# Kernel tuning notes

Hardware: AMD Instinct MI355X
Metric: run time of the kernel (lower is better)

Reference implementation:

```python
import jax, jax.numpy as jnp
import numpy as np

B, N = 4, 1024            # batches, atoms per structure
IN_CH, OUT_CH = 16, 16
N_BASIS = 16
MAX_RADIUS = 3.5
BOX_L = 19.7              # cubic lattice constant -> ~24 neighbors/atom
GAMMA = MAX_RADIUS / N_BASIS
N_NORM = 24.0             # avg neighbor count, out /= sqrt(n_norm)


def _build_periodic_edges(seed=0):
    rng = np.random.default_rng(seed)
    pos = rng.uniform(0.0, BOX_L, (B, N, 3)).astype(np.float32)
    shifts = BOX_L * np.array([[i, j, k] for i in (-1, 0, 1)
                               for j in (-1, 0, 1) for k in (-1, 0, 1)],
                              dtype=np.float32)
    src_l, dst_l, vec_l = [], [], []
    r2 = MAX_RADIUS * MAX_RADIUS
    for z in range(B):
        p = pos[z]
        for s in shifts:  # 27 periodic images, chunked to keep memory small
            diff = (p[None, :, :] + s[None, None, :]) - p[:, None, :]  # [a,b,3] = image_b - a
            d2 = (diff * diff).sum(-1)
            a_idx, b_idx = np.nonzero(d2 < r2)
            dst_l.append((z * N + a_idx).astype(np.int32))
            src_l.append((z * N + b_idx).astype(np.int32))
            vec_l.append(diff[a_idx, b_idx])
    edge_src = np.concatenate(src_l)
    edge_dst = np.concatenate(dst_l)
    edge_vec = np.concatenate(vec_l).astype(np.float32)
    # original zeroes self-image displacements with |r| < 1e-10
    self_mask = np.linalg.norm(edge_vec, axis=-1) < 1e-10
    edge_vec[self_mask] = 0.0
    return edge_src, edge_dst, edge_vec


def setup_inputs() -> dict:
    key = jax.random.key(0)
    k1, k2 = jax.random.split(key)
    edge_src, edge_dst, edge_vec = _build_periodic_edges()
    x = jax.random.normal(k1, (B * N, IN_CH), dtype=jnp.float32)
    W = jax.random.normal(k2, (N_BASIS + 3, OUT_CH, IN_CH), dtype=jnp.float32) * 0.1
    return {
        "x": x,
        "W": W,
        "edge_vec": jnp.asarray(edge_vec),
        "edge_src": jnp.asarray(edge_src),
        "edge_dst": jnp.asarray(edge_dst),
    }


def reference(x, W, edge_vec, edge_src, edge_dst):
    # per-edge kernel features: gaussian radial basis + unit direction
    r = jnp.linalg.norm(edge_vec, axis=-1, keepdims=True)            # [E,1]
    centers = jnp.linspace(0.0, MAX_RADIUS, N_BASIS, dtype=x.dtype)
    basis = jnp.exp(-((r - centers) / GAMMA) ** 2)                   # [E,nb]
    rhat = jnp.where(r > 1e-10, edge_vec / jnp.maximum(r, 1e-10), 0.0)
    feat = jnp.concatenate([basis, rhat], axis=-1)                   # [E,nb+3]
    # per-edge kernel eval (kernels = self.kernel(radius) in the original)
    K = jnp.einsum('ef,foi->eoi', feat, W)                           # [E,out,in]
    # per-edge matvec + scatter-add over destination atoms
    msg = jnp.einsum('eoi,ei->eo', K, x[edge_src])                   # [E,out]
    out = jax.ops.segment_sum(msg, edge_dst, num_segments=x.shape[0])
    out = out / jnp.sqrt(jnp.asarray(N_NORM, x.dtype))               # n_norm ** 0.5
    return out.reshape(B, N, OUT_CH)
```

## Files before the change

kernel.cpp:

```cpp
#include <hip/hip_runtime.h>
#include <math.h>

#define IN_CH 16
#define OUT_CH 16
#define N_BASIS 16
#define N_FEAT 19
#define Y_STRIDE (N_FEAT * OUT_CH)
#define GAMMA_INV (16.0f / 3.5f)
#define CENTER_STEP (3.5f / 15.0f)
#define INV_SQRT_NNORM 0.20412414523193154f

__global__ __launch_bounds__(320) void precompute_y(
    const float* __restrict__ x, const float* __restrict__ W,
    float* __restrict__ y, float* __restrict__ out, int n_atoms) {
  __shared__ float xs[IN_CH];
  const int a = blockIdx.x;
  const int t = threadIdx.x;
  if (t < IN_CH) {
    xs[t] = x[a * IN_CH + t];
    out[a * OUT_CH + t] = 0.0f;
  }
  __syncthreads();
  if (t < Y_STRIDE) {
    const float4* w4 = (const float4*)(W + t * IN_CH);
    float acc = 0.f;
#pragma unroll
    for (int q = 0; q < 4; ++q) {
      float4 w = w4[q];
      acc += w.x * xs[4 * q + 0] + w.y * xs[4 * q + 1] +
             w.z * xs[4 * q + 2] + w.w * xs[4 * q + 3];
    }
    y[(size_t)a * Y_STRIDE + t] = acc;
  }
}

__global__ __launch_bounds__(256) void edge_scatter(
    const float* __restrict__ y, const float* __restrict__ edge_vec,
    const int* __restrict__ edge_src, const int* __restrict__ edge_dst,
    float* __restrict__ out, int E) {
  __shared__ float feat[16][N_FEAT];
  __shared__ float msg[16][OUT_CH];
  __shared__ int dsts[16];

  const int t = threadIdx.x;
  const int eg = t >> 4;
  const int o = t & 15;
  const int e = blockIdx.x * 16 + eg;
  const bool valid = (e < E);

  float vx = 0.f, vy = 0.f, vz = 0.f;
  int src = 0;
  if (valid) {
    vx = edge_vec[3 * e + 0];
    vy = edge_vec[3 * e + 1];
    vz = edge_vec[3 * e + 2];
    src = edge_src[e];
    if (o == 0) dsts[eg] = edge_dst[e];
  } else if (o == 0) {
    dsts[eg] = -1 - eg;
  }
  const float r = sqrtf(vx * vx + vy * vy + vz * vz);

  const float tt = (r - CENTER_STEP * (float)o) * GAMMA_INV;
  feat[eg][o] = __expf(-tt * tt);
  if (o < 3) {
    const float inv = (r > 1e-10f) ? (1.0f / r) : 0.0f;
    const float comp = (o == 0) ? vx : ((o == 1) ? vy : vz);
    feat[eg][N_BASIS + o] = comp * inv;
  }
  __syncthreads();

  float acc = 0.f;
  if (valid) {
    const float* __restrict__ yrow = y + (size_t)src * Y_STRIDE + o;
#pragma unroll
    for (int f = 0; f < N_FEAT; ++f) acc += feat[eg][f] * yrow[f * OUT_CH];
  }
  msg[eg][o] = acc;
  __syncthreads();

  const int mydst = dsts[eg];
  int leader = eg;
#pragma unroll
  for (int j = 0; j < 16; ++j) {
    if (dsts[j] == mydst) { leader = j; break; }
  }
  if (leader == eg && mydst >= 0) {
    float total = 0.f;
#pragma unroll
    for (int j = 0; j < 16; ++j) {
      if (j >= eg && dsts[j] == mydst) total += msg[j][o];
    }
    atomicAdd(&out[mydst * OUT_CH + o], total * INV_SQRT_NNORM);
  }
}

__global__ __launch_bounds__(256) void edge_direct(
    const float* __restrict__ x, const float* __restrict__ W,
    const float* __restrict__ edge_vec, const int* __restrict__ edge_src,
    const int* __restrict__ edge_dst, float* __restrict__ out, int E) {
  __shared__ float Ws[N_FEAT * OUT_CH * IN_CH];
  __shared__ float feat[16][N_FEAT];
  __shared__ float xs[16][IN_CH];

  const int t = threadIdx.x;
  for (int i = t; i < N_FEAT * OUT_CH * IN_CH; i += 256) Ws[i] = W[i];

  const int eg = t >> 4;
  const int o = t & 15;
  const int e = blockIdx.x * 16 + eg;
  const bool valid = (e < E);

  float vx = 0.f, vy = 0.f, vz = 0.f;
  int src = 0, dst = 0;
  if (valid) {
    vx = edge_vec[3 * e + 0];
    vy = edge_vec[3 * e + 1];
    vz = edge_vec[3 * e + 2];
    src = edge_src[e];
    dst = edge_dst[e];
    xs[eg][o] = x[src * IN_CH + o];
  }
  const float r = sqrtf(vx * vx + vy * vy + vz * vz);
  const float tt = (r - CENTER_STEP * (float)o) * GAMMA_INV;
  feat[eg][o] = __expf(-tt * tt);
  if (o < 3) {
    const float inv = (r > 1e-10f) ? (1.0f / r) : 0.0f;
    const float comp = (o == 0) ? vx : ((o == 1) ? vy : vz);
    feat[eg][N_BASIS + o] = comp * inv;
  }
  __syncthreads();

  if (valid) {
    float acc = 0.f;
#pragma unroll
    for (int f = 0; f < N_FEAT; ++f) {
      const float* wrow = &Ws[(f * OUT_CH + o) * IN_CH];
      float dot = 0.f;
#pragma unroll
      for (int i = 0; i < IN_CH; ++i) dot += wrow[i] * xs[eg][i];
      acc += feat[eg][f] * dot;
    }
    atomicAdd(&out[dst * OUT_CH + o], acc * INV_SQRT_NNORM);
  }
}

extern "C" void kernel_launch(void* const* d_in, const int* in_sizes, int n_in,
                              void* d_out, int out_size, void* d_ws,
                              size_t ws_size, hipStream_t stream) {
  const float* x = (const float*)d_in[0];
  const float* W = (const float*)d_in[1];
  const float* edge_vec = (const float*)d_in[2];
  const int* edge_src = (const int*)d_in[3];
  const int* edge_dst = (const int*)d_in[4];
  float* out = (float*)d_out;

  const int E = in_sizes[3];
  const int n_atoms = in_sizes[0] / IN_CH;

  const size_t y_bytes = (size_t)n_atoms * Y_STRIDE * sizeof(float);
  const int edge_blocks = (E + 15) / 16;
  if (ws_size >= y_bytes) {
    float* y = (float*)d_ws;
    precompute_y<<<n_atoms, 320, 0, stream>>>(x, W, y, out, n_atoms);
    edge_scatter<<<edge_blocks, 256, 0, stream>>>(y, edge_vec, edge_src,
                                                  edge_dst, out, E);
  } else {
    hipMemsetAsync(out, 0, (size_t)out_size * sizeof(float), stream);
    edge_direct<<<edge_blocks, 256, 0, stream>>>(x, W, edge_vec, edge_src,
                                                 edge_dst, out, E);
  }
}
```

Before: 83.84 us.

## Transpose y to feature-contiguous padded layout and process 64 edges per block

Changes the precomputed per-atom y table from [feat][out] to [out][feat padded to 20], so each output thread reads its 19 feature coefficients as five float4 loads. The edge kernel now handles 64 edges per 256-thread block with coalesced staging of edge vectors and indices in shared memory. The scatter reduction merges consecutive runs of equal destination within the larger tile, so fewer atomics are issued. The cost is a y table that is about 5% larger and more shared memory per block. The run-merge loop assumes edges are grouped by destination to get the full atomic reduction.

```diff
diff --git a/kernel.cpp b/kernel.cpp
--- a/kernel.cpp
+++ b/kernel.cpp
@@ -5,14 +5,16 @@
 #define OUT_CH 16
 #define N_BASIS 16
 #define N_FEAT 19
-#define Y_STRIDE (N_FEAT * OUT_CH)
+#define YF 20
+#define Y_STRIDE (OUT_CH * YF)
 #define GAMMA_INV (16.0f / 3.5f)
 #define CENTER_STEP (3.5f / 15.0f)
 #define INV_SQRT_NNORM 0.20412414523193154f
+#define EPB 64
 
 __global__ __launch_bounds__(320) void precompute_y(
     const float* __restrict__ x, const float* __restrict__ W,
-    float* __restrict__ y, float* __restrict__ out, int n_atoms) {
+    float* __restrict__ y, float* __restrict__ out) {
   __shared__ float xs[IN_CH];
   const int a = blockIdx.x;
   const int t = threadIdx.x;
@@ -21,77 +23,94 @@
     out[a * OUT_CH + t] = 0.0f;
   }
   __syncthreads();
-  if (t < Y_STRIDE) {
-    const float4* w4 = (const float4*)(W + t * IN_CH);
-    float acc = 0.f;
+  const int o = t / YF;
+  const int f = t % YF;
+  float acc = 0.f;
+  if (f < N_FEAT) {
+    const float4* w4 = (const float4*)(W + (f * OUT_CH + o) * IN_CH);
 #pragma unroll
     for (int q = 0; q < 4; ++q) {
       float4 w = w4[q];
       acc += w.x * xs[4 * q + 0] + w.y * xs[4 * q + 1] +
              w.z * xs[4 * q + 2] + w.w * xs[4 * q + 3];
     }
-    y[(size_t)a * Y_STRIDE + t] = acc;
   }
+  y[(size_t)a * Y_STRIDE + t] = acc;
 }
 
 __global__ __launch_bounds__(256) void edge_scatter(
     const float* __restrict__ y, const float* __restrict__ edge_vec,
     const int* __restrict__ edge_src, const int* __restrict__ edge_dst,
     float* __restrict__ out, int E) {
-  __shared__ float feat[16][N_FEAT];
-  __shared__ float msg[16][OUT_CH];
-  __shared__ int dsts[16];
+  __shared__ float ev[EPB * 3];
+  __shared__ int srcs[EPB];
+  __shared__ int dsts[EPB];
+  __shared__ float feat[EPB][YF];
+  __shared__ float msg[EPB][OUT_CH];
 
   const int t = threadIdx.x;
-  const int eg = t >> 4;
-  const int o = t & 15;
-  const int e = blockIdx.x * 16 + eg;
-  const bool valid = (e < E);
+  const int e0 = blockIdx.x * EPB;
 
-  float vx = 0.f, vy = 0.f, vz = 0.f;
-  int src = 0;
-  if (valid) {
-    vx = edge_vec[3 * e + 0];
-    vy = edge_vec[3 * e + 1];
-    vz = edge_vec[3 * e + 2];
-    src = edge_src[e];
-    if (o == 0) dsts[eg] = edge_dst[e];
-  } else if (o == 0) {
-    dsts[eg] = -1 - eg;
+  if (t < EPB * 3) {
+    const int idx = e0 * 3 + t;
+    ev[t] = (idx < E * 3) ? edge_vec[idx] : 0.0f;
   }
-  const float r = sqrtf(vx * vx + vy * vy + vz * vz);
-
-  const float tt = (r - CENTER_STEP * (float)o) * GAMMA_INV;
-  feat[eg][o] = __expf(-tt * tt);
-  if (o < 3) {
-    const float inv = (r > 1e-10f) ? (1.0f / r) : 0.0f;
-    const float comp = (o == 0) ? vx : ((o == 1) ? vy : vz);
-    feat[eg][N_BASIS + o] = comp * inv;
+  if (t < EPB) {
+    srcs[t] = (e0 + t < E) ? edge_src[e0 + t] : 0;
+  } else if (t < 2 * EPB) {
+    const int s = t - EPB;
+    dsts[s] = (e0 + s < E) ? edge_dst[e0 + s] : (-1 - s);
   }
   __syncthreads();
 
-  float acc = 0.f;
-  if (valid) {
-    const float* __restrict__ yrow = y + (size_t)src * Y_STRIDE + o;
+  const int g = t >> 4;
+  const int o = t & 15;
+
 #pragma unroll
-    for (int f = 0; f < N_FEAT; ++f) acc += feat[eg][f] * yrow[f * OUT_CH];
+  for (int j = 0; j < 4; ++j) {
+    const int s = g + 16 * j;
+    const float vx = ev[3 * s + 0], vy = ev[3 * s + 1], vz = ev[3 * s + 2];
+    const float r = sqrtf(vx * vx + vy * vy + vz * vz);
+    const float tt = (r - CENTER_STEP * (float)o) * GAMMA_INV;
+    feat[s][o] = __expf(-tt * tt);
+    if (o < 3) {
+      const float inv = (r > 1e-10f) ? (1.0f / r) : 0.0f;
+      const float comp = (o == 0) ? vx : ((o == 1) ? vy : vz);
+      feat[s][N_BASIS + o] = comp * inv;
+    }
+    if (o == 3) feat[s][N_FEAT] = 0.0f;
   }
-  msg[eg][o] = acc;
   __syncthreads();
 
-  const int mydst = dsts[eg];
-  int leader = eg;
 #pragma unroll
-  for (int j = 0; j < 16; ++j) {
-    if (dsts[j] == mydst) { leader = j; break; }
+  for (int j = 0; j < 4; ++j) {
+    const int s = g + 16 * j;
+    float acc = 0.f;
+    if (e0 + s < E) {
+      const float4* yr = (const float4*)(y + ((size_t)srcs[s] * OUT_CH + o) * YF);
+      const float4* fr = (const float4*)(&feat[s][0]);
+#pragma unroll
+      for (int q = 0; q < 5; ++q) {
+        float4 yv = yr[q];
+        float4 fv = fr[q];
+        acc += yv.x * fv.x + yv.y * fv.y + yv.z * fv.z + yv.w * fv.w;
+      }
+    }
+    msg[s][o] = acc;
   }
-  if (leader == eg && mydst >= 0) {
-    float total = 0.f;
+  __syncthreads();
+
 #pragma unroll
-    for (int j = 0; j < 16; ++j) {
-      if (j >= eg && dsts[j] == mydst) total += msg[j][o];
+  for (int j = 0; j < 4; ++j) {
+    const int s = g + 16 * j;
+    const int d = dsts[s];
+    const bool tail = (s == EPB - 1) || (dsts[s + 1] != d);
+    if (tail && d >= 0) {
+      float tot = 0.f;
+      int q = s;
+      while (q >= 0 && dsts[q] == d) { tot += msg[q][o]; --q; }
+      atomicAdd(&out[d * OUT_CH + o], tot * INV_SQRT_NNORM);
     }
-    atomicAdd(&out[mydst * OUT_CH + o], total * INV_SQRT_NNORM);
   }
 }
 
@@ -159,15 +178,14 @@
   const int n_atoms = in_sizes[0] / IN_CH;
 
   const size_t y_bytes = (size_t)n_atoms * Y_STRIDE * sizeof(float);
-  const int edge_blocks = (E + 15) / 16;
   if (ws_size >= y_bytes) {
     float* y = (float*)d_ws;
-    precompute_y<<<n_atoms, 320, 0, stream>>>(x, W, y, out, n_atoms);
-    edge_scatter<<<edge_blocks, 256, 0, stream>>>(y, edge_vec, edge_src,
-                                                  edge_dst, out, E);
+    precompute_y<<<n_atoms, 320, 0, stream>>>(x, W, y, out);
+    edge_scatter<<<(E + EPB - 1) / EPB, 256, 0, stream>>>(y, edge_vec, edge_src,
+                                                          edge_dst, out, E);
   } else {
     hipMemsetAsync(out, 0, (size_t)out_size * sizeof(float), stream);
-    edge_direct<<<edge_blocks, 256, 0, stream>>>(x, W, edge_vec, edge_src,
-                                                 edge_dst, out, E);
+    edge_direct<<<(E + 15) / 16, 256, 0, stream>>>(x, W, edge_vec, edge_src,
+                                                   edge_dst, out, E);
   }
 }
```

Result: slower. 91.49 us (+9.1%).
